# Kernel tuning notes

Measured on AMD Instinct MI355X. Metric: run time of the kernel, lower is better.

Reference implementation:

```python
import jax, jax.numpy as jnp
import numpy as np

B = 128          # batch of independent QP instances
N = 512          # n_assets
N_ITERS = 500    # accelerated projected-gradient iterations (converges tightly)
POWER_ITERS = 30 # power iterations for Lipschitz estimate


def setup_inputs() -> dict:
    key = jax.random.key(0)
    k1, k2 = jax.random.split(key)
    mu = 0.1 * jax.random.normal(k1, (B, N), dtype=jnp.float32)
    # Sigma must be symmetric PSD for cp.quad_form to define a convex QP
    A = jax.random.normal(k2, (B, N, N), dtype=jnp.float32)
    Sigma = jnp.einsum('bik,bjk->bij', A, A) / N + 1e-3 * jnp.eye(N, dtype=jnp.float32)
    return {"mu": mu, "Sigma": Sigma}


def _project_simplex(v):
    # Euclidean projection of each row of v onto {w : sum w = 1, w >= 0}
    n = v.shape[-1]
    u = jnp.sort(v, axis=-1)[..., ::-1]                    # descending
    css = jnp.cumsum(u, axis=-1) - 1.0
    ind = jnp.arange(1, n + 1, dtype=v.dtype)
    rho = jnp.sum(u - css / ind > 0, axis=-1, keepdims=True)  # >= 1
    theta = jnp.take_along_axis(css, rho - 1, axis=-1) / rho.astype(v.dtype)
    return jnp.maximum(v - theta, 0.0)


def _solve_qp(mu, Sigma):
    # minimize w^T Sigma w - mu^T w  s.t.  sum w = 1, w >= 0
    Sigma = 0.5 * (Sigma + jnp.swapaxes(Sigma, -1, -2))  # quad_form assumes symmetric

    # Lipschitz constant of grad: 2*lambda_max(Sigma), via power iteration
    b = jnp.ones((Sigma.shape[0], Sigma.shape[-1]), dtype=mu.dtype) / Sigma.shape[-1]
    def power_step(b, _):
        Sb = jnp.einsum('bij,bj->bi', Sigma, b)
        b = Sb / (jnp.linalg.norm(Sb, axis=-1, keepdims=True) + 1e-12)
        return b, None
    b, _ = jax.lax.scan(power_step, b, None, length=POWER_ITERS)
    lmax = jnp.einsum('bi,bij,bj->b', b, Sigma, b)[:, None]  # [B,1]
    step = 1.0 / (2.0 * lmax + 1e-8)

    # Accelerated projected gradient (FISTA) on the simplex
    w0 = jnp.ones_like(mu) / mu.shape[-1]
    def fista_step(carry, _):
        w, y, t = carry
        g = 2.0 * jnp.einsum('bij,bj->bi', Sigma, y) - mu
        w_new = _project_simplex(y - step * g)
        t_new = 0.5 * (1.0 + jnp.sqrt(1.0 + 4.0 * t * t))
        y_new = w_new + ((t - 1.0) / t_new) * (w_new - w)
        return (w_new, y_new, t_new), None
    (w, _, _), _ = jax.lax.scan(fista_step, (w0, w0, jnp.float32(1.0)), None, length=N_ITERS)
    return w


def reference(mu, Sigma):
    return _solve_qp(mu, Sigma)
```

## Files before the change

### kernel.cpp

```cpp
#include <hip/hip_runtime.h>
#include <hip/hip_fp16.h>
#include <math.h>

#define BATCH 128
#define NDIM 512
#define NPAIR 256
#define POWER_ITERS 30
#define N_ITERS 500
#define KEEP 40
#define LDSP 16
#define STRM 8

typedef _Float16 half2_t __attribute__((ext_vector_type(2)));

union H2x4 { float4 f4; half2_t h[4]; };

__device__ __forceinline__ float4 ld4(const float* p) { return *(const float4*)p; }
__device__ __forceinline__ float4 f4_add(float4 a, float4 b) {
  return make_float4(a.x + b.x, a.y + b.y, a.z + b.z, a.w + b.w);
}
__device__ __forceinline__ float wave_sum64(float x) {
#pragma unroll
  for (int off = 1; off < 64; off <<= 1) x += __shfl_xor(x, off, 64);
  return x;
}
__device__ __forceinline__ float wave_max64(float x) {
#pragma unroll
  for (int off = 1; off < 64; off <<= 1) x = fmaxf(x, __shfl_xor(x, off, 64));
  return x;
}
__device__ __forceinline__ void fd4(float4 sv, half2_t yy,
                                    float& a0, float& a1, float& a2, float& a3) {
  H2x4 s; s.f4 = sv;
  a0 = __builtin_amdgcn_fdot2(s.h[0], yy, a0, false);
  a1 = __builtin_amdgcn_fdot2(s.h[1], yy, a1, false);
  a2 = __builtin_amdgcn_fdot2(s.h[2], yy, a2, false);
  a3 = __builtin_amdgcn_fdot2(s.h[3], yy, a3, false);
}

__global__ void sym_conv_kernel(const float* __restrict__ S, half2_t* __restrict__ Sh) {
  const int bb = blockIdx.x, ti = blockIdx.y, tj = blockIdx.z;
  if (tj < ti) return;
  __shared__ float ta[32][33];
  __shared__ float tb[32][33];
  const float* base = S + (size_t)bb * NDIM * NDIM;
  half2_t* dst = Sh + (size_t)bb * NPAIR * NDIM;
  const int tx = threadIdx.x, ty = threadIdx.y;
#pragma unroll
  for (int k = 0; k < 4; k++) {
    int r = ty + 8 * k;
    ta[r][tx] = base[(size_t)(ti * 32 + r) * NDIM + tj * 32 + tx];
    tb[r][tx] = base[(size_t)(tj * 32 + r) * NDIM + ti * 32 + tx];
  }
  __syncthreads();
#pragma unroll
  for (int k = 0; k < 2; k++) {
    int pi = ty + 8 * k;
    float v0 = 0.5f * (ta[2 * pi][tx] + tb[tx][2 * pi]);
    float v1 = 0.5f * (ta[2 * pi + 1][tx] + tb[tx][2 * pi + 1]);
    half2_t o; o[0] = (_Float16)v0; o[1] = (_Float16)v1;
    dst[(size_t)(ti * 16 + pi) * NDIM + tj * 32 + tx] = o;
  }
  if (ti != tj) {
#pragma unroll
    for (int k = 0; k < 2; k++) {
      int pi = ty + 8 * k;
      float v0 = 0.5f * (tb[2 * pi][tx] + ta[tx][2 * pi]);
      float v1 = 0.5f * (tb[2 * pi + 1][tx] + ta[tx][2 * pi + 1]);
      half2_t o; o[0] = (_Float16)v0; o[1] = (_Float16)v1;
      dst[(size_t)(tj * 16 + pi) * NDIM + ti * 32 + tx] = o;
    }
  }
}

__device__ __forceinline__ void combine_z(const float* __restrict__ zsc, int lane, float* z8) {
#pragma unroll
  for (int q = 0; q < 2; q++) {
    float4 zz = ld4(zsc + 0 * NDIM + 8 * lane + 4 * q);
    zz = f4_add(zz, ld4(zsc + 1 * NDIM + 8 * lane + 4 * q));
    zz = f4_add(zz, ld4(zsc + 2 * NDIM + 8 * lane + 4 * q));
    zz = f4_add(zz, ld4(zsc + 3 * NDIM + 8 * lane + 4 * q));
    z8[4 * q + 0] = zz.x; z8[4 * q + 1] = zz.y;
    z8[4 * q + 2] = zz.z; z8[4 * q + 3] = zz.w;
  }
}

__device__ __forceinline__ void store_y_pairs(half2_t* ysh, int lane, const float* y8) {
  H2x4 yo;
#pragma unroll
  for (int q = 0; q < 4; q++) {
    half2_t v; v[0] = (_Float16)y8[2 * q]; v[1] = (_Float16)y8[2 * q + 1];
    yo.h[q] = v;
  }
  *(float4*)(ysh + 4 * lane) = yo.f4;
}

__global__ __attribute__((amdgpu_flat_work_group_size(512, 512)))
__attribute__((amdgpu_waves_per_eu(2)))
void qp_solver_h(const float* __restrict__ mu,
                 const half2_t* __restrict__ Sh,
                 float* __restrict__ out) {
  __shared__ __align__(16) float4 lsm[4 * LDSP][128];
  __shared__ __align__(16) half2_t yh2[NPAIR];
  __shared__ __align__(16) float zsc[4 * NDIM];
  __shared__ int stopf;
  const int tid = threadIdx.x;
  const int g = tid >> 7;
  const int c = tid & 127;
  const int b = blockIdx.x;
  const half2_t* Sb = Sh + (size_t)b * NPAIR * NDIM;
  const float invn = 1.0f / (float)NDIM;
  const half2_t* rp = Sb + (size_t)(64 * g) * NDIM + 4 * c;
  const half2_t* gp = rp + (size_t)(KEEP + LDSP) * NDIM;

  float4 sreg[KEEP];
#pragma unroll
  for (int p = 0; p < KEEP; p++) sreg[p] = *(const float4*)(rp + (size_t)p * NDIM);
#pragma unroll
  for (int k = 0; k < LDSP; k++)
    lsm[g * LDSP + k][c] = *(const float4*)(rp + (size_t)(KEEP + k) * NDIM);

  if (tid < NPAIR) { half2_t v; v[0] = (_Float16)invn; v[1] = (_Float16)invn; yh2[tid] = v; }
  if (tid == 0) stopf = 0;

  float y8[8], w8[8], mu8[8];
  float t = 1.0f, step = 0.f, maxinc = 0.f;
  float th = -3e38f;
  if (tid < 64) {
    float4 m0 = ld4(mu + (size_t)b * NDIM + 8 * tid);
    float4 m1 = ld4(mu + (size_t)b * NDIM + 8 * tid + 4);
    mu8[0] = m0.x; mu8[1] = m0.y; mu8[2] = m0.z; mu8[3] = m0.w;
    mu8[4] = m1.x; mu8[5] = m1.y; mu8[6] = m1.z; mu8[7] = m1.w;
#pragma unroll
    for (int k = 0; k < 8; k++) { y8[k] = invn; w8[k] = invn; }
  }
  __syncthreads();

  const int TOT = POWER_ITERS + 1 + N_ITERS;
  for (int it = 0; it < TOT; it++) {
    float a0 = 0.f, a1 = 0.f, a2 = 0.f, a3 = 0.f;
    {
      const half2_t* ybase = yh2 + 64 * g;
      float4 stA[STRM];
#pragma unroll
      for (int k = 0; k < STRM; k++) stA[k] = *(const float4*)(gp + (size_t)k * NDIM);
#pragma unroll
      for (int ch = 0; ch < KEEP / 4; ch++) {
        H2x4 y4; y4.f4 = *(const float4*)(ybase + 4 * ch);
#pragma unroll
        for (int q = 0; q < 4; q++) fd4(sreg[4 * ch + q], y4.h[q], a0, a1, a2, a3);
      }
#pragma unroll
      for (int k = 0; k < LDSP; k++)
        fd4(lsm[g * LDSP + k][c], ybase[KEEP + k], a0, a1, a2, a3);
#pragma unroll
      for (int k = 0; k < STRM; k++) fd4(stA[k], ybase[KEEP + LDSP + k], a0, a1, a2, a3);
    }
    *(float4*)(zsc + g * NDIM + 4 * c) = make_float4(a0, a1, a2, a3);
    __syncthreads();

    if (tid < 64) {
      float z8[8];
      combine_z(zsc, tid, z8);
      if (it < POWER_ITERS) {
        float ss = 0.f;
#pragma unroll
        for (int k = 0; k < 8; k++) ss += z8[k] * z8[k];
        ss = wave_sum64(ss);
        float inv = 1.0f / (sqrtf(ss) + 1e-12f);
#pragma unroll
        for (int k = 0; k < 8; k++) y8[k] = z8[k] * inv;
        store_y_pairs(yh2, tid, y8);
      } else if (it == POWER_ITERS) {
        float dd = 0.f;
#pragma unroll
        for (int k = 0; k < 8; k++) dd += z8[k] * y8[k];
        dd = wave_sum64(dd);
        step = 1.0f / (2.0f * dd + 1e-8f);
#pragma unroll
        for (int k = 0; k < 8; k++) { y8[k] = invn; w8[k] = invn; }
        t = 1.0f; maxinc = 0.f;
        store_y_pairs(yh2, tid, y8);
      } else {
        float v8[8];
#pragma unroll
        for (int k = 0; k < 8; k++)
          v8[k] = y8[k] - step * (2.0f * z8[k] - mu8[k]);

        {
          float s = 0.f, cn = 0.f, stot = 0.f;
#pragma unroll
          for (int k = 0; k < 8; k++) {
            stot += v8[k];
            if (v8[k] > th) { s += v8[k]; cn += 1.f; }
          }
#pragma unroll
          for (int off = 1; off < 64; off <<= 1) {
            s    += __shfl_xor(s, off, 64);
            cn   += __shfl_xor(cn, off, 64);
            stot += __shfl_xor(stot, off, 64);
          }
          th = (cn > 0.f) ? (s - 1.0f) / cn
                          : (stot - 1.0f) * (1.0f / 512.0f);
        }
        for (int m = 0; m < 16; m++) {
          float s = 0.f, cn = 0.f;
#pragma unroll
          for (int k = 0; k < 8; k++)
            if (v8[k] > th) { s += v8[k]; cn += 1.f; }
#pragma unroll
          for (int off = 1; off < 64; off <<= 1) {
            s  += __shfl_xor(s, off, 64);
            cn += __shfl_xor(cn, off, 64);
          }
          float thn = (s - 1.0f) / cn;
          if (!(thn > th)) break;
          th = thn;
        }

        float tn = 0.5f * (1.0f + sqrtf(1.0f + 4.0f * t * t));
        float coef = (t - 1.0f) / tn;
#pragma unroll
        for (int k = 0; k < 8; k++) {
          float wn = fmaxf(v8[k] - th, 0.0f);
          maxinc = fmaxf(maxinc, fabsf(wn - w8[k]));
          y8[k] = wn + coef * (wn - w8[k]);
          w8[k] = wn;
        }
        t = tn;
        store_y_pairs(yh2, tid, y8);
        if ((it & 3) == 3) {
          float mi = wave_max64(maxinc);
          if (tid == 0) stopf = (mi < 1e-7f) ? (stopf + 1) : 0;
          maxinc = 0.f;
        }
      }
    }
    __syncthreads();
    if (stopf >= 2) break;
  }

  if (tid < 64) {
    *(float4*)(out + (size_t)b * NDIM + 8 * tid)     = make_float4(w8[0], w8[1], w8[2], w8[3]);
    *(float4*)(out + (size_t)b * NDIM + 8 * tid + 4) = make_float4(w8[4], w8[5], w8[6], w8[7]);
  }
}

__global__ void symmetrize_kernel(float* __restrict__ S) {
  const int ti = blockIdx.y, tj = blockIdx.z;
  if (tj < ti) return;
  __shared__ float ta[32][33];
  __shared__ float tb[32][33];
  float* base = S + (size_t)blockIdx.x * NDIM * NDIM;
  const int tx = threadIdx.x, ty = threadIdx.y;
#pragma unroll
  for (int k = 0; k < 4; k++) {
    int r = ty + 8 * k;
    ta[r][tx] = base[(size_t)(ti * 32 + r) * NDIM + tj * 32 + tx];
    tb[r][tx] = base[(size_t)(tj * 32 + r) * NDIM + ti * 32 + tx];
  }
  __syncthreads();
#pragma unroll
  for (int k = 0; k < 4; k++) {
    int r = ty + 8 * k;
    base[(size_t)(ti * 32 + r) * NDIM + tj * 32 + tx] = 0.5f * (ta[r][tx] + tb[tx][r]);
  }
#pragma unroll
  for (int k = 0; k < 4; k++) {
    int r = ty + 8 * k;
    base[(size_t)(tj * 32 + r) * NDIM + ti * 32 + tx] = 0.5f * (tb[r][tx] + ta[tx][r]);
  }
}

__device__ __forceinline__ float4 f4_fma(float4 a, float s, float4 acc) {
  acc.x = fmaf(a.x, s, acc.x); acc.y = fmaf(a.y, s, acc.y);
  acc.z = fmaf(a.z, s, acc.z); acc.w = fmaf(a.w, s, acc.w);
  return acc;
}
__device__ __forceinline__ void matvec_partial(const float* __restrict__ Sb,
                                               const float* __restrict__ yv,
                                               float* __restrict__ zsc, int g, int c) {
  const float* rp = Sb + (size_t)(g * 128) * NDIM + 4 * c;
  const float* yp = yv + g * 128;
  float4 a0 = make_float4(0, 0, 0, 0), a1 = a0, a2 = a0, a3 = a0;
#pragma unroll 4
  for (int m = 0; m < 32; m++) {
    float4 yq = ld4(yp + 4 * m);
    float4 s0 = ld4(rp + (size_t)(4 * m + 0) * NDIM);
    float4 s1 = ld4(rp + (size_t)(4 * m + 1) * NDIM);
    float4 s2 = ld4(rp + (size_t)(4 * m + 2) * NDIM);
    float4 s3 = ld4(rp + (size_t)(4 * m + 3) * NDIM);
    a0 = f4_fma(s0, yq.x, a0); a1 = f4_fma(s1, yq.y, a1);
    a2 = f4_fma(s2, yq.z, a2); a3 = f4_fma(s3, yq.w, a3);
  }
  float4 z = f4_add(f4_add(a0, a1), f4_add(a2, a3));
  *(float4*)(zsc + g * NDIM + 4 * c) = z;
}

__launch_bounds__(512, 1)
__global__ void qp_solver(const float* __restrict__ mu,
                          const float* __restrict__ S,
                          float* __restrict__ out) {
  __shared__ float yv[NDIM];
  __shared__ float zsc[4 * NDIM];
  __shared__ float bc[1];
  const int tid = threadIdx.x, g = tid >> 7, c = tid & 127, b = blockIdx.x;
  const float* Sb = S + (size_t)b * NDIM * NDIM;
  const float invn = 1.0f / (float)NDIM;
  yv[tid] = invn;
  __syncthreads();
  for (int it = 0; it < POWER_ITERS; it++) {
    matvec_partial(Sb, yv, zsc, g, c);
    __syncthreads();
    if (tid < 64) {
      float z8[8]; combine_z(zsc, tid, z8);
      float ss = 0.f;
#pragma unroll
      for (int k = 0; k < 8; k++) ss += z8[k] * z8[k];
      ss = wave_sum64(ss);
      float inv = 1.0f / (sqrtf(ss) + 1e-12f);
      *(float4*)(yv + 8 * tid)     = make_float4(z8[0]*inv, z8[1]*inv, z8[2]*inv, z8[3]*inv);
      *(float4*)(yv + 8 * tid + 4) = make_float4(z8[4]*inv, z8[5]*inv, z8[6]*inv, z8[7]*inv);
    }
    __syncthreads();
  }
  matvec_partial(Sb, yv, zsc, g, c);
  __syncthreads();
  if (tid < 64) {
    float z8[8]; combine_z(zsc, tid, z8);
    float dd = 0.f;
#pragma unroll
    for (int k = 0; k < 8; k++) dd += z8[k] * yv[8 * tid + k];
    dd = wave_sum64(dd);
    if (tid == 0) bc[0] = 1.0f / (2.0f * dd + 1e-8f);
  }
  __syncthreads();
  const float step = bc[0];
  yv[tid] = invn;
  float w8[8], y8[8], mu8[8];
  if (tid < 64) {
#pragma unroll
    for (int k = 0; k < 8; k++) { w8[k] = invn; y8[k] = invn; }
    float4 m0 = ld4(mu + (size_t)b * NDIM + 8 * tid);
    float4 m1 = ld4(mu + (size_t)b * NDIM + 8 * tid + 4);
    mu8[0] = m0.x; mu8[1] = m0.y; mu8[2] = m0.z; mu8[3] = m0.w;
    mu8[4] = m1.x; mu8[5] = m1.y; mu8[6] = m1.z; mu8[7] = m1.w;
  }
  __syncthreads();
  float t = 1.0f;
  for (int it = 0; it < N_ITERS; it++) {
    matvec_partial(Sb, yv, zsc, g, c);
    __syncthreads();
    if (tid < 64) {
      float z8[8], v8[8]; combine_z(zsc, tid, z8);
#pragma unroll
      for (int k = 0; k < 8; k++) v8[k] = y8[k] - step * (2.0f * z8[k] - mu8[k]);
      float th = -1e30f;
      for (int m = 0; m < 64; m++) {
        float s = 0.f, cn = 0.f;
#pragma unroll
        for (int k = 0; k < 8; k++) if (v8[k] > th) { s += v8[k]; cn += 1.f; }
#pragma unroll
        for (int off = 1; off < 64; off <<= 1) { s += __shfl_xor(s, off, 64); cn += __shfl_xor(cn, off, 64); }
        float thn = (s - 1.0f) / cn;
        if (!(thn > th)) break;
        th = thn;
      }
      float tn = 0.5f * (1.0f + sqrtf(1.0f + 4.0f * t * t));
      float coef = (t - 1.0f) / tn;
#pragma unroll
      for (int k = 0; k < 8; k++) {
        float wn = fmaxf(v8[k] - th, 0.0f);
        y8[k] = wn + coef * (wn - w8[k]);
        w8[k] = wn;
      }
      *(float4*)(yv + 8 * tid)     = make_float4(y8[0], y8[1], y8[2], y8[3]);
      *(float4*)(yv + 8 * tid + 4) = make_float4(y8[4], y8[5], y8[6], y8[7]);
      t = tn;
    }
    __syncthreads();
  }
  if (tid < 64) {
    *(float4*)(out + (size_t)b * NDIM + 8 * tid)     = make_float4(w8[0], w8[1], w8[2], w8[3]);
    *(float4*)(out + (size_t)b * NDIM + 8 * tid + 4) = make_float4(w8[4], w8[5], w8[6], w8[7]);
  }
}

extern "C" void kernel_launch(void* const* d_in, const int* in_sizes, int n_in,
                              void* d_out, int out_size, void* d_ws, size_t ws_size,
                              hipStream_t stream) {
  const float* mu = (const float*)d_in[0];
  float* Sg = (float*)d_in[1];
  if (n_in >= 2 && in_sizes[0] > in_sizes[1]) { mu = (const float*)d_in[1]; Sg = (float*)d_in[0]; }
  float* out = (float*)d_out;

  const size_t need = (size_t)BATCH * NPAIR * NDIM * sizeof(half2_t);
  if (ws_size >= need) {
    half2_t* Sh = (half2_t*)d_ws;
    sym_conv_kernel<<<dim3(BATCH, 16, 16), dim3(32, 8), 0, stream>>>(Sg, Sh);
    qp_solver_h<<<dim3(BATCH), dim3(512), 0, stream>>>(mu, Sh, out);
  } else {
    symmetrize_kernel<<<dim3(BATCH, 16, 16), dim3(32, 8), 0, stream>>>(Sg);
    qp_solver<<<dim3(BATCH), dim3(512), 0, stream>>>(mu, Sg, out);
  }
}
```

Measured before the change: 1.715 ms.

## Keep Sigma rows in AGPRs, rotate streamed loads, use LDS-only barriers

```diff
diff --git a/kernel.cpp b/kernel.cpp
--- a/kernel.cpp
+++ b/kernel.cpp
@@ -7,7 +7,8 @@
 #define NPAIR 256
 #define POWER_ITERS 30
 #define N_ITERS 500
-#define KEEP 40
+#define AGP 32
+#define VK 8
 #define LDSP 16
 #define STRM 8
 
@@ -37,6 +38,12 @@
   a2 = __builtin_amdgcn_fdot2(s.h[2], yy, a2, false);
   a3 = __builtin_amdgcn_fdot2(s.h[3], yy, a3, false);
 }
+
+#define BAR_LDS() do {                                        \
+    asm volatile("s_waitcnt lgkmcnt(0)" ::: "memory");        \
+    __builtin_amdgcn_s_barrier();                             \
+    asm volatile("" ::: "memory");                            \
+  } while (0)
 
 __global__ void sym_conv_kernel(const float* __restrict__ S, half2_t* __restrict__ Sh) {
   const int bb = blockIdx.x, ti = blockIdx.y, tj = blockIdx.z;
@@ -111,14 +118,27 @@
   const half2_t* Sb = Sh + (size_t)b * NPAIR * NDIM;
   const float invn = 1.0f / (float)NDIM;
   const half2_t* rp = Sb + (size_t)(64 * g) * NDIM + 4 * c;
-  const half2_t* gp = rp + (size_t)(KEEP + LDSP) * NDIM;
-
-  float4 sreg[KEEP];
-#pragma unroll
-  for (int p = 0; p < KEEP; p++) sreg[p] = *(const float4*)(rp + (size_t)p * NDIM);
+  const half2_t* gp = rp + (size_t)(AGP + VK + LDSP) * NDIM;
+
+  float ag[4 * AGP];
+#pragma unroll
+  for (int p = 0; p < AGP; p++) {
+    float4 v = *(const float4*)(rp + (size_t)p * NDIM);
+    asm("v_accvgpr_write_b32 %0, %1" : "=a"(ag[4 * p + 0]) : "v"(v.x));
+    asm("v_accvgpr_write_b32 %0, %1" : "=a"(ag[4 * p + 1]) : "v"(v.y));
+    asm("v_accvgpr_write_b32 %0, %1" : "=a"(ag[4 * p + 2]) : "v"(v.z));
+    asm("v_accvgpr_write_b32 %0, %1" : "=a"(ag[4 * p + 3]) : "v"(v.w));
+  }
+  float4 sreg[VK];
+#pragma unroll
+  for (int p = 0; p < VK; p++)
+    sreg[p] = *(const float4*)(rp + (size_t)(AGP + p) * NDIM);
 #pragma unroll
   for (int k = 0; k < LDSP; k++)
-    lsm[g * LDSP + k][c] = *(const float4*)(rp + (size_t)(KEEP + k) * NDIM);
+    lsm[g * LDSP + k][c] = *(const float4*)(rp + (size_t)(AGP + VK + k) * NDIM);
+  float4 stA[STRM];
+#pragma unroll
+  for (int k = 0; k < STRM; k++) stA[k] = *(const float4*)(gp + (size_t)k * NDIM);
 
   if (tid < NPAIR) { half2_t v; v[0] = (_Float16)invn; v[1] = (_Float16)invn; yh2[tid] = v; }
   if (tid == 0) stopf = 0;
@@ -141,23 +161,41 @@
     float a0 = 0.f, a1 = 0.f, a2 = 0.f, a3 = 0.f;
     {
       const half2_t* ybase = yh2 + 64 * g;
-      float4 stA[STRM];
+#pragma unroll
+      for (int k = 0; k < STRM; k++)
+        fd4(stA[k], ybase[AGP + VK + LDSP + k], a0, a1, a2, a3);
 #pragma unroll
       for (int k = 0; k < STRM; k++) stA[k] = *(const float4*)(gp + (size_t)k * NDIM);
 #pragma unroll
-      for (int ch = 0; ch < KEEP / 4; ch++) {
+      for (int ch = 0; ch < AGP / 4; ch++) {
         H2x4 y4; y4.f4 = *(const float4*)(ybase + 4 * ch);
 #pragma unroll
+        for (int q = 0; q < 4; q++) {
+          int p = 4 * ch + q;
+          float x0, x1, x2, x3;
+          asm("v_accvgpr_read_b32 %0, %1" : "=v"(x0) : "a"(ag[4 * p + 0]));
+          asm("v_accvgpr_read_b32 %0, %1" : "=v"(x1) : "a"(ag[4 * p + 1]));
+          asm("v_accvgpr_read_b32 %0, %1" : "=v"(x2) : "a"(ag[4 * p + 2]));
+          asm("v_accvgpr_read_b32 %0, %1" : "=v"(x3) : "a"(ag[4 * p + 3]));
+          fd4(make_float4(x0, x1, x2, x3), y4.h[q], a0, a1, a2, a3);
+        }
+      }
+#pragma unroll
+      for (int ch = 0; ch < VK / 4; ch++) {
+        H2x4 y4; y4.f4 = *(const float4*)(ybase + AGP + 4 * ch);
+#pragma unroll
         for (int q = 0; q < 4; q++) fd4(sreg[4 * ch + q], y4.h[q], a0, a1, a2, a3);
       }
 #pragma unroll
-      for (int k = 0; k < LDSP; k++)
-        fd4(lsm[g * LDSP + k][c], ybase[KEEP + k], a0, a1, a2, a3);
-#pragma unroll
-      for (int k = 0; k < STRM; k++) fd4(stA[k], ybase[KEEP + LDSP + k], a0, a1, a2, a3);
+      for (int ch = 0; ch < LDSP / 4; ch++) {
+        H2x4 y4; y4.f4 = *(const float4*)(ybase + AGP + VK + 4 * ch);
+#pragma unroll
+        for (int q = 0; q < 4; q++)
+          fd4(lsm[g * LDSP + 4 * ch + q][c], y4.h[q], a0, a1, a2, a3);
+      }
     }
     *(float4*)(zsc + g * NDIM + 4 * c) = make_float4(a0, a1, a2, a3);
-    __syncthreads();
+    BAR_LDS();
 
     if (tid < 64) {
       float z8[8];
@@ -236,7 +274,7 @@
         }
       }
     }
-    __syncthreads();
+    BAR_LDS();
     if (stopf >= 2) break;
   }
 
```

New measurement: 2.309 ms. 1.35x slower.

## Double solver block to 1024 threads, splitting matvec rows across eight groups

Applied to the files above, without the earlier changes.

```diff
diff --git a/kernel.cpp b/kernel.cpp
--- a/kernel.cpp
+++ b/kernel.cpp
@@ -7,8 +7,8 @@
 #define NPAIR 256
 #define POWER_ITERS 30
 #define N_ITERS 500
-#define KEEP 40
-#define LDSP 16
+#define REGK 16
+#define LDSP 8
 #define STRM 8
 
 typedef _Float16 half2_t __attribute__((ext_vector_type(2)));
@@ -73,13 +73,13 @@
   }
 }
 
-__device__ __forceinline__ void combine_z(const float* __restrict__ zsc, int lane, float* z8) {
+__device__ __forceinline__ void combine_z8(const float* __restrict__ zsc, int lane, float* z8) {
 #pragma unroll
   for (int q = 0; q < 2; q++) {
-    float4 zz = ld4(zsc + 0 * NDIM + 8 * lane + 4 * q);
-    zz = f4_add(zz, ld4(zsc + 1 * NDIM + 8 * lane + 4 * q));
-    zz = f4_add(zz, ld4(zsc + 2 * NDIM + 8 * lane + 4 * q));
-    zz = f4_add(zz, ld4(zsc + 3 * NDIM + 8 * lane + 4 * q));
+    float4 zz = ld4(zsc + 8 * lane + 4 * q);
+#pragma unroll
+    for (int gg = 1; gg < 8; gg++)
+      zz = f4_add(zz, ld4(zsc + gg * NDIM + 8 * lane + 4 * q));
     z8[4 * q + 0] = zz.x; z8[4 * q + 1] = zz.y;
     z8[4 * q + 2] = zz.z; z8[4 * q + 3] = zz.w;
   }
@@ -95,14 +95,13 @@
   *(float4*)(ysh + 4 * lane) = yo.f4;
 }
 
-__global__ __attribute__((amdgpu_flat_work_group_size(512, 512)))
-__attribute__((amdgpu_waves_per_eu(2)))
+__global__ __launch_bounds__(1024)
 void qp_solver_h(const float* __restrict__ mu,
                  const half2_t* __restrict__ Sh,
                  float* __restrict__ out) {
-  __shared__ __align__(16) float4 lsm[4 * LDSP][128];
+  __shared__ __align__(16) float4 lsm[8 * LDSP][128];
   __shared__ __align__(16) half2_t yh2[NPAIR];
-  __shared__ __align__(16) float zsc[4 * NDIM];
+  __shared__ __align__(16) float zsc[8 * NDIM];
   __shared__ int stopf;
   const int tid = threadIdx.x;
   const int g = tid >> 7;
@@ -110,27 +109,23 @@
   const int b = blockIdx.x;
   const half2_t* Sb = Sh + (size_t)b * NPAIR * NDIM;
   const float invn = 1.0f / (float)NDIM;
-  const half2_t* rp = Sb + (size_t)(64 * g) * NDIM + 4 * c;
-  const half2_t* gp = rp + (size_t)(KEEP + LDSP) * NDIM;
-
-  float4 sreg[KEEP];
-#pragma unroll
-  for (int p = 0; p < KEEP; p++) sreg[p] = *(const float4*)(rp + (size_t)p * NDIM);
+  const half2_t* rp = Sb + (size_t)(32 * g) * NDIM + 4 * c;
+  const half2_t* gp = rp + (size_t)(REGK + LDSP) * NDIM;
+
+  float4 sreg[REGK];
+#pragma unroll
+  for (int p = 0; p < REGK; p++) sreg[p] = *(const float4*)(rp + (size_t)p * NDIM);
 #pragma unroll
   for (int k = 0; k < LDSP; k++)
-    lsm[g * LDSP + k][c] = *(const float4*)(rp + (size_t)(KEEP + k) * NDIM);
+    lsm[g * LDSP + k][c] = *(const float4*)(rp + (size_t)(REGK + k) * NDIM);
 
   if (tid < NPAIR) { half2_t v; v[0] = (_Float16)invn; v[1] = (_Float16)invn; yh2[tid] = v; }
   if (tid == 0) stopf = 0;
 
-  float y8[8], w8[8], mu8[8];
+  float y8[8], w8[8];
   float t = 1.0f, step = 0.f, maxinc = 0.f;
   float th = -3e38f;
   if (tid < 64) {
-    float4 m0 = ld4(mu + (size_t)b * NDIM + 8 * tid);
-    float4 m1 = ld4(mu + (size_t)b * NDIM + 8 * tid + 4);
-    mu8[0] = m0.x; mu8[1] = m0.y; mu8[2] = m0.z; mu8[3] = m0.w;
-    mu8[4] = m1.x; mu8[5] = m1.y; mu8[6] = m1.z; mu8[7] = m1.w;
 #pragma unroll
     for (int k = 0; k < 8; k++) { y8[k] = invn; w8[k] = invn; }
   }
@@ -140,28 +135,55 @@
   for (int it = 0; it < TOT; it++) {
     float a0 = 0.f, a1 = 0.f, a2 = 0.f, a3 = 0.f;
     {
-      const half2_t* ybase = yh2 + 64 * g;
-      float4 stA[STRM];
-#pragma unroll
-      for (int k = 0; k < STRM; k++) stA[k] = *(const float4*)(gp + (size_t)k * NDIM);
-#pragma unroll
-      for (int ch = 0; ch < KEEP / 4; ch++) {
+      const half2_t* ybase = yh2 + 32 * g;
+      float4 stA[4], stB[4];
+#pragma unroll
+      for (int k = 0; k < 4; k++) stA[k] = *(const float4*)(gp + (size_t)k * NDIM);
+#pragma unroll
+      for (int ch = 0; ch < 2; ch++) {
         H2x4 y4; y4.f4 = *(const float4*)(ybase + 4 * ch);
 #pragma unroll
         for (int q = 0; q < 4; q++) fd4(sreg[4 * ch + q], y4.h[q], a0, a1, a2, a3);
       }
 #pragma unroll
-      for (int k = 0; k < LDSP; k++)
-        fd4(lsm[g * LDSP + k][c], ybase[KEEP + k], a0, a1, a2, a3);
-#pragma unroll
-      for (int k = 0; k < STRM; k++) fd4(stA[k], ybase[KEEP + LDSP + k], a0, a1, a2, a3);
+      for (int k = 0; k < 4; k++) stB[k] = *(const float4*)(gp + (size_t)(4 + k) * NDIM);
+#pragma unroll
+      for (int ch = 2; ch < 4; ch++) {
+        H2x4 y4; y4.f4 = *(const float4*)(ybase + 4 * ch);
+#pragma unroll
+        for (int q = 0; q < 4; q++) fd4(sreg[4 * ch + q], y4.h[q], a0, a1, a2, a3);
+      }
+      {
+        H2x4 y4; y4.f4 = *(const float4*)(ybase + REGK + LDSP);
+#pragma unroll
+        for (int k = 0; k < 4; k++) fd4(stA[k], y4.h[k], a0, a1, a2, a3);
+      }
+#pragma unroll
+      for (int ch = 0; ch < 2; ch++) {
+        H2x4 y4; y4.f4 = *(const float4*)(ybase + REGK + 4 * ch);
+#pragma unroll
+        for (int q = 0; q < 4; q++)
+          fd4(lsm[g * LDSP + 4 * ch + q][c], y4.h[q], a0, a1, a2, a3);
+      }
+      {
+        H2x4 y4; y4.f4 = *(const float4*)(ybase + REGK + LDSP + 4);
+#pragma unroll
+        for (int k = 0; k < 4; k++) fd4(stB[k], y4.h[k], a0, a1, a2, a3);
+      }
     }
     *(float4*)(zsc + g * NDIM + 4 * c) = make_float4(a0, a1, a2, a3);
     __syncthreads();
 
     if (tid < 64) {
+      float mu8[8];
+      if (it > POWER_ITERS) {
+        float4 m0 = ld4(mu + (size_t)b * NDIM + 8 * tid);
+        float4 m1 = ld4(mu + (size_t)b * NDIM + 8 * tid + 4);
+        mu8[0] = m0.x; mu8[1] = m0.y; mu8[2] = m0.z; mu8[3] = m0.w;
+        mu8[4] = m1.x; mu8[5] = m1.y; mu8[6] = m1.z; mu8[7] = m1.w;
+      }
       float z8[8];
-      combine_z(zsc, tid, z8);
+      combine_z8(zsc, tid, z8);
       if (it < POWER_ITERS) {
         float ss = 0.f;
 #pragma unroll
@@ -276,6 +298,17 @@
   acc.x = fmaf(a.x, s, acc.x); acc.y = fmaf(a.y, s, acc.y);
   acc.z = fmaf(a.z, s, acc.z); acc.w = fmaf(a.w, s, acc.w);
   return acc;
+}
+__device__ __forceinline__ void combine_z(const float* __restrict__ zsc, int lane, float* z8) {
+#pragma unroll
+  for (int q = 0; q < 2; q++) {
+    float4 zz = ld4(zsc + 0 * NDIM + 8 * lane + 4 * q);
+    zz = f4_add(zz, ld4(zsc + 1 * NDIM + 8 * lane + 4 * q));
+    zz = f4_add(zz, ld4(zsc + 2 * NDIM + 8 * lane + 4 * q));
+    zz = f4_add(zz, ld4(zsc + 3 * NDIM + 8 * lane + 4 * q));
+    z8[4 * q + 0] = zz.x; z8[4 * q + 1] = zz.y;
+    z8[4 * q + 2] = zz.z; z8[4 * q + 3] = zz.w;
+  }
 }
 __device__ __forceinline__ void matvec_partial(const float* __restrict__ Sb,
                                                const float* __restrict__ yv,
@@ -398,7 +431,7 @@
   if (ws_size >= need) {
     half2_t* Sh = (half2_t*)d_ws;
     sym_conv_kernel<<<dim3(BATCH, 16, 16), dim3(32, 8), 0, stream>>>(Sg, Sh);
-    qp_solver_h<<<dim3(BATCH), dim3(512), 0, stream>>>(mu, Sh, out);
+    qp_solver_h<<<dim3(BATCH), dim3(1024), 0, stream>>>(mu, Sh, out);
   } else {
     symmetrize_kernel<<<dim3(BATCH, 16, 16), dim3(32, 8), 0, stream>>>(Sg);
     qp_solver<<<dim3(BATCH), dim3(512), 0, stream>>>(mu, Sg, out);
```

New measurement: 2.952 ms. +72.1%, slower.
